# Optimization experiments

Measured on AMD Instinct MI355X. Metric: run time of the kernel, lower is better.

Reference implementation:

```python
import jax, jax.numpy as jnp
import numpy as np

K_STEPS = 10
ALPHA = 0.9
N_NODES = 16384
N_CLASSES = 64
N_EDGES = 524288


def setup_inputs() -> dict:
    key = jax.random.key(0)
    k1, k2, k3 = jax.random.split(key, 3)
    masked_y_true = jax.random.normal(k1, (N_NODES, N_CLASSES), dtype=jnp.float32)
    K = jax.random.normal(k2, (N_NODES, N_NODES), dtype=jnp.float32)
    edge_index = jax.random.randint(k3, (2, N_EDGES), 0, N_NODES, dtype=jnp.int32)
    return {"masked_y_true": masked_y_true, "K": K, "edge_index": edge_index}


def reference(masked_y_true, K, edge_index):
    src, dst = edge_index[0], edge_index[1]
    # DAD normalization: w_e = deg(src)^-1/2 * deg(dst)^-1/2
    deg = jnp.zeros((N_NODES,), jnp.float32).at[dst].add(1.0)
    dinv = jax.lax.rsqrt(jnp.maximum(deg, 1.0))
    w = dinv[src] * dinv[dst]  # [E]

    def spmm(x):
        # A @ x with A in edge-list form (static sparsity, reused each step)
        return jax.ops.segment_sum(w[:, None] * x[src], dst, num_segments=N_NODES)

    def prop_step(_, y):
        return ALPHA * spmm(y) + (1.0 - ALPHA) * y

    y = jax.lax.fori_loop(0, K_STEPS, prop_step, masked_y_true)
    y = K @ y
    y = jax.lax.fori_loop(0, K_STEPS, prop_step, y)
    return y
```

## Files before the change

### kernel.cpp

```cpp
#include <hip/hip_runtime.h>

#define NN 16384
#define NC 64
#define NE 524288
#define ALPHA 0.9f
#define KSTEPS 10

typedef _Float16 f16;
typedef _Float16 f16x4 __attribute__((ext_vector_type(4)));
typedef _Float16 f16x8 __attribute__((ext_vector_type(8)));
typedef float f32x4 __attribute__((ext_vector_type(4)));
typedef int i32x16 __attribute__((ext_vector_type(16)));

#define MEMB   asm volatile("" ::: "memory")
#define SCHED0 __builtin_amdgcn_sched_barrier(0)

__global__ __launch_bounds__(256) void deg_kernel(const int* __restrict__ dst,
                                                  unsigned* __restrict__ deg) {
    int e = blockIdx.x * 256 + threadIdx.x;
    atomicAdd(&deg[dst[e]], 1u);
}

__global__ __launch_bounds__(1024) void scan_kernel(const unsigned* __restrict__ deg,
                                                    float* __restrict__ dinv,
                                                    unsigned* __restrict__ rowoff,
                                                    unsigned* __restrict__ cursor) {
    __shared__ unsigned part[1024];
    const int t = threadIdx.x;
    const int base = t * 16;
    unsigned local[16];
    unsigned s = 0;
    #pragma unroll
    for (int i = 0; i < 16; ++i) {
        local[i] = s;
        s += (deg[base + i] + 15u) & ~15u;
    }
    part[t] = s;
    __syncthreads();
    for (int off = 1; off < 1024; off <<= 1) {
        unsigned v = (t >= off) ? part[t - off] : 0u;
        __syncthreads();
        part[t] += v;
        __syncthreads();
    }
    const unsigned ex = (t == 0) ? 0u : part[t - 1];
    #pragma unroll
    for (int i = 0; i < 16; ++i) {
        unsigned ro = ex + local[i];
        rowoff[base + i] = ro;
        cursor[base + i] = ro;
        unsigned d = deg[base + i];
        dinv[base + i] = rsqrtf(fmaxf((float)d, 1.0f));
    }
    if (t == 1023) rowoff[NN] = part[1023];
}

__global__ __launch_bounds__(256) void fill_kernel(const int* __restrict__ src,
                                                   const int* __restrict__ dst,
                                                   const float* __restrict__ dinv,
                                                   unsigned* __restrict__ cursor,
                                                   int2* __restrict__ csr) {
    int e = blockIdx.x * 256 + threadIdx.x;
    int s = src[e], d = dst[e];
    float w = dinv[s] * dinv[d];
    unsigned p = atomicAdd(&cursor[d], 1u);
    csr[p] = make_int2(s, __float_as_int(w));
}

__global__ __launch_bounds__(256) void prop_kernel(const float* __restrict__ x,
                                                   float* __restrict__ y,
                                                   const unsigned* __restrict__ rowoff,
                                                   const int* __restrict__ csr) {
    const int lane = threadIdx.x & 63;
    const int n = __builtin_amdgcn_readfirstlane(blockIdx.x * 4 + (threadIdx.x >> 6));
    const unsigned beg = rowoff[n];
    const unsigned np = (rowoff[n + 1] - beg) >> 4;
    float acc0 = 0.f, acc1 = 0.f;
    if (np) {
        i32x16 e0 = *(const i32x16*)(csr + 2 * beg);
        i32x16 e1 = *(const i32x16*)(csr + 2 * beg + 16);
        float xv0[8], xv1[8];
        #pragma unroll
        for (int j = 0; j < 8; ++j) xv0[j] = x[(unsigned)e0[2 * j] * 64u + lane];
        #pragma unroll
        for (int j = 0; j < 8; ++j) xv1[j] = x[(unsigned)e1[2 * j] * 64u + lane];
        for (unsigned p = 1; p < np; ++p) {
            const i32x16 f0 = *(const i32x16*)(csr + 2 * (beg + p * 16));
            const i32x16 f1 = *(const i32x16*)(csr + 2 * (beg + p * 16) + 16);
            #pragma unroll
            for (int j = 0; j < 8; ++j) {
                const float w = __int_as_float(e0[2 * j + 1]);
                if (j & 1) acc1 = fmaf(w, xv0[j], acc1);
                else       acc0 = fmaf(w, xv0[j], acc0);
            }
            #pragma unroll
            for (int j = 0; j < 8; ++j) xv0[j] = x[(unsigned)f0[2 * j] * 64u + lane];
            #pragma unroll
            for (int j = 0; j < 8; ++j) {
                const float w = __int_as_float(e1[2 * j + 1]);
                if (j & 1) acc1 = fmaf(w, xv1[j], acc1);
                else       acc0 = fmaf(w, xv1[j], acc0);
            }
            #pragma unroll
            for (int j = 0; j < 8; ++j) xv1[j] = x[(unsigned)f1[2 * j] * 64u + lane];
            e0 = f0; e1 = f1;
        }
        #pragma unroll
        for (int j = 0; j < 8; ++j) {
            const float w = __int_as_float(e0[2 * j + 1]);
            if (j & 1) acc1 = fmaf(w, xv0[j], acc1);
            else       acc0 = fmaf(w, xv0[j], acc0);
        }
        #pragma unroll
        for (int j = 0; j < 8; ++j) {
            const float w = __int_as_float(e1[2 * j + 1]);
            if (j & 1) acc1 = fmaf(w, xv1[j], acc1);
            else       acc0 = fmaf(w, xv1[j], acc0);
        }
    }
    y[n * 64 + lane] = ALPHA * (acc0 + acc1) + (1.0f - ALPHA) * x[n * 64 + lane];
}

__global__ __launch_bounds__(256) void ysplit_kernel(const float* __restrict__ y,
                                                     f16* __restrict__ yhT,
                                                     f16* __restrict__ ylT) {
    __shared__ f16 hb[64][72];
    __shared__ f16 lb[64][72];
    const int t = threadIdx.x;
    const int b = blockIdx.x;
    const int kl = t >> 2;
    const int cq = (t & 3) * 16;
    #pragma unroll
    for (int i = 0; i < 4; ++i) {
        float4 v = *(const float4*)&y[(size_t)(b * 64 + kl) * 64 + cq + i * 4];
        float vv[4] = {v.x, v.y, v.z, v.w};
        #pragma unroll
        for (int j = 0; j < 4; ++j) {
            int c = cq + i * 4 + j;
            f16 h = (f16)vv[j];
            float r = vv[j] - (float)h;
            hb[c][kl] = h;
            lb[c][kl] = (f16)r;
        }
    }
    __syncthreads();
    const int c = t >> 2;
    const int kq = (t & 3) * 16;
    #pragma unroll
    for (int s2 = 0; s2 < 2; ++s2) {
        int slot = (kq >> 3) + s2;
        int dslot = slot ^ (c & 7);
        f16x8 hv, lv;
        #pragma unroll
        for (int j = 0; j < 8; ++j) { hv[j] = hb[c][kq + s2 * 8 + j]; lv[j] = lb[c][kq + s2 * 8 + j]; }
        *(f16x8*)&yhT[(size_t)c * NN + b * 64 + dslot * 8] = hv;
        *(f16x8*)&ylT[(size_t)c * NN + b * 64 + dslot * 8] = lv;
    }
}

__device__ inline void gload16(const void* g, void* l) {
    __builtin_amdgcn_global_load_lds((const __attribute__((address_space(1))) void*)g,
                                     (__attribute__((address_space(3))) void*)l, 16, 0, 0);
}

#define AH_OFF 0
#define AL_OFF 16384
#define YP_OFF 32768

__global__ __launch_bounds__(256, 2) void gemm_kernel(const float* __restrict__ A,
                                                      const f16* __restrict__ yhT,
                                                      const f16* __restrict__ ylT,
                                                      float* __restrict__ z) {
    __shared__ char lds[65536];
    const int t = threadIdx.x;
    const int w = t >> 6;
    const int l = t & 63;
    const size_t row0 = (size_t)blockIdx.x * 128;
    const int kbase = blockIdx.y * 2048;
    const int stag = (blockIdx.x + blockIdx.y * 4) & 31;

    f32x4 acc[2][4];
    #pragma unroll
    for (int m = 0; m < 2; ++m)
        #pragma unroll
        for (int n = 0; n < 4; ++n)
            acc[m][n] = (f32x4){0.f, 0.f, 0.f, 0.f};

    const int arow_l = w * 4 + (l >> 4);
    const int acol = (l & 15) * 4;
    const int ycr = l >> 3;
    const int yco = (l & 7) * 8;

    float4 aA[8], aB[8];

    auto tmap = [&](int tile) { return (stag + tile) & 31; };

    auto loadA = [&](float4 (&dst)[8], int tile) {
        const int kt = kbase + tmap(tile) * 64;
        #pragma unroll
        for (int i = 0; i < 8; ++i)
            dst[i] = *(const float4*)&A[(row0 + i * 16 + arow_l) * 16384 + kt + acol];
    };
    auto issueY = [&](int tile, int cur) {
        const int kt = kbase + tmap(tile) * 64;
        #pragma unroll
        for (int j = 0; j < 2; ++j) {
            const int i = 2 * w + j;
            gload16(yhT + (size_t)(i * 8 + ycr) * NN + kt + yco,
                    lds + YP_OFF + cur * 16384 + i * 1024);
            gload16(ylT + (size_t)(i * 8 + ycr) * NN + kt + yco,
                    lds + YP_OFF + cur * 16384 + 8192 + i * 1024);
        }
    };
    auto writeA = [&](const float4 (&src)[8]) {
        #pragma unroll
        for (int i = 0; i < 8; ++i) {
            const int r = i * 16 + arow_l;
            float v[4] = {src[i].x, src[i].y, src[i].z, src[i].w};
            f16x4 h4, l4;
            #pragma unroll
            for (int j = 0; j < 4; ++j) {
                f16 h = (f16)v[j];
                h4[j] = h;
                l4[j] = (f16)(v[j] - (float)h);
            }
            const int byte = r * 128 + (((((l & 15) >> 1)) ^ (r & 7)) << 4) + (l & 1) * 8;
            *(f16x4*)(lds + AH_OFF + byte) = h4;
            *(f16x4*)(lds + AL_OFF + byte) = l4;
        }
    };
    auto mfmaTile = [&](int cur) {
        #pragma unroll
        for (int s = 0; s < 2; ++s) {
            const int slot = s * 4 + (l >> 4);
            f16x8 ah[2], alo[2];
            #pragma unroll
            for (int m = 0; m < 2; ++m) {
                const int r = w * 32 + m * 16 + (l & 15);
                const int byte = r * 128 + ((slot ^ (r & 7)) << 4);
                ah[m]  = *(const f16x8*)(lds + AH_OFF + byte);
                alo[m] = *(const f16x8*)(lds + AL_OFF + byte);
            }
            #pragma unroll
            for (int n = 0; n < 4; ++n) {
                const int c = n * 16 + (l & 15);
                const int byte = c * 128 + ((slot ^ (c & 7)) << 4);
                const f16x8 bh = *(const f16x8*)(lds + YP_OFF + cur * 16384 + byte);
                const f16x8 bl = *(const f16x8*)(lds + YP_OFF + cur * 16384 + 8192 + byte);
                #pragma unroll
                for (int m = 0; m < 2; ++m) {
                    acc[m][n] = __builtin_amdgcn_mfma_f32_16x16x32_f16(ah[m],  bh, acc[m][n], 0, 0, 0);
                    acc[m][n] = __builtin_amdgcn_mfma_f32_16x16x32_f16(ah[m],  bl, acc[m][n], 0, 0, 0);
                    acc[m][n] = __builtin_amdgcn_mfma_f32_16x16x32_f16(alo[m], bh, acc[m][n], 0, 0, 0);
                }
            }
        }
    };

    loadA(aA, 0); MEMB;
    issueY(0, 0); MEMB;
    loadA(aB, 1); MEMB;
    writeA(aA);
    asm volatile("s_waitcnt vmcnt(8)" ::: "memory");  SCHED0;
    asm volatile("s_waitcnt lgkmcnt(0)" ::: "memory"); SCHED0;
    __builtin_amdgcn_s_barrier(); SCHED0;

#define GEMM_ITER(TILE, CUR, SETF, SETW)                                      \
    issueY((TILE) + 1, (CUR) ^ 1); MEMB;                                      \
    loadA(SETF, (TILE) + 2); MEMB;                                            \
    mfmaTile(CUR);                                                            \
    MEMB; SCHED0;                                                             \
    __builtin_amdgcn_s_barrier();                 \
    writeA(SETW);                                  \
    asm volatile("s_waitcnt vmcnt(8)" ::: "memory");  SCHED0;   \
    asm volatile("s_waitcnt lgkmcnt(0)" ::: "memory"); SCHED0;                \
    __builtin_amdgcn_s_barrier(); SCHED0;

    for (int tp = 0; tp < 15; ++tp) {
        const int t0 = 2 * tp;
        GEMM_ITER(t0,     0, aA, aB);
        GEMM_ITER(t0 + 1, 1, aB, aA);
    }
    issueY(31, 1); MEMB;
    mfmaTile(0);
    MEMB; SCHED0;
    __builtin_amdgcn_s_barrier();
    writeA(aB);
    asm volatile("s_waitcnt vmcnt(0)" ::: "memory");  SCHED0;
    asm volatile("s_waitcnt lgkmcnt(0)" ::: "memory"); SCHED0;
    __builtin_amdgcn_s_barrier(); SCHED0;
    mfmaTile(1);
#undef GEMM_ITER

    #pragma unroll
    for (int m = 0; m < 2; ++m)
        #pragma unroll
        for (int n = 0; n < 4; ++n)
            #pragma unroll
            for (int q = 0; q < 4; ++q) {
                const size_t gr = row0 + w * 32 + m * 16 + (l >> 4) * 4 + q;
                const int gc = n * 16 + (l & 15);
                atomicAdd(&z[gr * 64 + gc], acc[m][n][q]);
            }
}

extern "C" void kernel_launch(void* const* d_in, const int* in_sizes, int n_in,
                              void* d_out, int out_size, void* d_ws, size_t ws_size,
                              hipStream_t stream) {
    const float* ytrue = (const float*)d_in[0];
    const float* Kmat  = (const float*)d_in[1];
    const int*   eidx  = (const int*)d_in[2];
    const int* esrc = eidx;
    const int* edst = eidx + NE;
    float* out = (float*)d_out;

    char* ws = (char*)d_ws;
    size_t off = 0;
    auto alloc = [&](size_t bytes) -> void* {
        void* p = ws + off;
        off += (bytes + 255) & ~(size_t)255;
        return p;
    };
    const size_t CSR_ENTRIES = (size_t)NE + 16 * NN;
    unsigned* deg    = (unsigned*)alloc((size_t)NN * 4);
    unsigned* rowoff = (unsigned*)alloc((size_t)(NN + 1) * 4);
    unsigned* cursor = (unsigned*)alloc((size_t)NN * 4);
    float*    dinv   = (float*)alloc((size_t)NN * 4);
    int2*     csr    = (int2*)alloc(CSR_ENTRIES * 8);
    float*    yA     = (float*)alloc((size_t)NN * NC * 4);
    float*    yB     = (float*)alloc((size_t)NN * NC * 4);
    f16*      yhT    = (f16*)alloc((size_t)NC * NN * 2);
    f16*      ylT    = (f16*)alloc((size_t)NC * NN * 2);

    hipMemsetAsync(deg, 0, (size_t)NN * 4, stream);
    hipMemsetAsync(csr, 0, CSR_ENTRIES * 8, stream);
    deg_kernel<<<NE / 256, 256, 0, stream>>>(edst, deg);
    scan_kernel<<<1, 1024, 0, stream>>>(deg, dinv, rowoff, cursor);
    fill_kernel<<<NE / 256, 256, 0, stream>>>(esrc, edst, dinv, cursor, csr);

    const float* cur = ytrue;
    float* bufs[2] = {yA, yB};
    int pb = 0;
    for (int s = 0; s < KSTEPS; ++s) {
        float* nxt = bufs[pb];
        pb ^= 1;
        prop_kernel<<<NN / 4, 256, 0, stream>>>(cur, nxt, rowoff, (const int*)csr);
        cur = nxt;
    }

    ysplit_kernel<<<NN / 64, 256, 0, stream>>>(cur, yhT, ylT);

    float* z = (cur == yA) ? yB : yA;
    hipMemsetAsync(z, 0, (size_t)NN * NC * 4, stream);
    gemm_kernel<<<dim3(128, 8), 256, 0, stream>>>(Kmat, yhT, ylT, z);

    float* other = (z == yA) ? yB : yA;
    const float* c2 = z;
    for (int s = 0; s < KSTEPS; ++s) {
        float* nxt = (s == KSTEPS - 1) ? out : other;
        prop_kernel<<<NN / 4, 256, 0, stream>>>(c2, nxt, rowoff, (const int*)csr);
        other = (float*)c2;
        c2 = nxt;
    }
}
```

Measured before the change: 522.1 us.

## Load A fragments directly into MFMA registers, skip LDS staging for A

Each wave now loads its own A rows straight from global memory in the MFMA fragment layout and splits fp32 into f16 hi/lo in registers, removing the LDS write/read round trip for A. Only the Y tiles stay in LDS, which halves shared memory use and allows raising the launch-bounds occupancy hint from 2 to 4 blocks. Waves no longer share A loads through LDS, so the per-thread global access pattern changes to 32-byte chunks per row, which may coalesce less well. Register pressure also shifts.

Measured after the change: 550.7 us. 1.05x slower.

```diff
diff --git a/kernel.cpp b/kernel.cpp
--- a/kernel.cpp
+++ b/kernel.cpp
@@ -163,15 +163,11 @@
                                      (__attribute__((address_space(3))) void*)l, 16, 0, 0);
 }
 
-#define AH_OFF 0
-#define AL_OFF 16384
-#define YP_OFF 32768
-
-__global__ __launch_bounds__(256, 2) void gemm_kernel(const float* __restrict__ A,
+__global__ __launch_bounds__(256, 4) void gemm_kernel(const float* __restrict__ A,
                                                       const f16* __restrict__ yhT,
                                                       const f16* __restrict__ ylT,
                                                       float* __restrict__ z) {
-    __shared__ char lds[65536];
+    __shared__ char lds[32768];
     const int t = threadIdx.x;
     const int w = t >> 6;
     const int l = t & 63;
@@ -186,67 +182,58 @@
         for (int n = 0; n < 4; ++n)
             acc[m][n] = (f32x4){0.f, 0.f, 0.f, 0.f};
 
-    const int arow_l = w * 4 + (l >> 4);
-    const int acol = (l & 15) * 4;
     const int ycr = l >> 3;
     const int yco = (l & 7) * 8;
-
-    float4 aA[8], aB[8];
+    const float* abase = A + (row0 + w * 32 + (l & 15)) * 16384 + (l >> 4) * 8;
+
+    float4 rA[2][2][2], rB[2][2][2];
 
     auto tmap = [&](int tile) { return (stag + tile) & 31; };
 
-    auto loadA = [&](float4 (&dst)[8], int tile) {
+    auto loadA = [&](float4 (&dst)[2][2][2], int tile) {
         const int kt = kbase + tmap(tile) * 64;
         #pragma unroll
-        for (int i = 0; i < 8; ++i)
-            dst[i] = *(const float4*)&A[(row0 + i * 16 + arow_l) * 16384 + kt + acol];
+        for (int m = 0; m < 2; ++m)
+            #pragma unroll
+            for (int s = 0; s < 2; ++s) {
+                const float* p = abase + (size_t)m * 16 * 16384 + kt + s * 32;
+                dst[m][s][0] = *(const float4*)p;
+                dst[m][s][1] = *(const float4*)(p + 4);
+            }
     };
-    auto issueY = [&](int tile, int cur) {
+    auto issueY = [&](int tile, int buf) {
         const int kt = kbase + tmap(tile) * 64;
         #pragma unroll
         for (int j = 0; j < 2; ++j) {
             const int i = 2 * w + j;
             gload16(yhT + (size_t)(i * 8 + ycr) * NN + kt + yco,
-                    lds + YP_OFF + cur * 16384 + i * 1024);
+                    lds + buf * 16384 + i * 1024);
             gload16(ylT + (size_t)(i * 8 + ycr) * NN + kt + yco,
-                    lds + YP_OFF + cur * 16384 + 8192 + i * 1024);
+                    lds + buf * 16384 + 8192 + i * 1024);
         }
     };
-    auto writeA = [&](const float4 (&src)[8]) {
-        #pragma unroll
-        for (int i = 0; i < 8; ++i) {
-            const int r = i * 16 + arow_l;
-            float v[4] = {src[i].x, src[i].y, src[i].z, src[i].w};
-            f16x4 h4, l4;
-            #pragma unroll
-            for (int j = 0; j < 4; ++j) {
-                f16 h = (f16)v[j];
-                h4[j] = h;
-                l4[j] = (f16)(v[j] - (float)h);
-            }
-            const int byte = r * 128 + (((((l & 15) >> 1)) ^ (r & 7)) << 4) + (l & 1) * 8;
-            *(f16x4*)(lds + AH_OFF + byte) = h4;
-            *(f16x4*)(lds + AL_OFF + byte) = l4;
-        }
-    };
-    auto mfmaTile = [&](int cur) {
+    auto mfmaTile = [&](const float4 (&raw)[2][2][2], int buf) {
         #pragma unroll
         for (int s = 0; s < 2; ++s) {
             const int slot = s * 4 + (l >> 4);
             f16x8 ah[2], alo[2];
             #pragma unroll
             for (int m = 0; m < 2; ++m) {
-                const int r = w * 32 + m * 16 + (l & 15);
-                const int byte = r * 128 + ((slot ^ (r & 7)) << 4);
-                ah[m]  = *(const f16x8*)(lds + AH_OFF + byte);
-                alo[m] = *(const f16x8*)(lds + AL_OFF + byte);
+                const float vv[8] = {raw[m][s][0].x, raw[m][s][0].y, raw[m][s][0].z, raw[m][s][0].w,
+                                     raw[m][s][1].x, raw[m][s][1].y, raw[m][s][1].z, raw[m][s][1].w};
+                #pragma unroll
+                for (int j = 0; j < 8; ++j) {
+                    f16 h = (f16)vv[j];
+                    ah[m][j] = h;
+                    alo[m][j] = (f16)(vv[j] - (float)h);
+                }
             }
             #pragma unroll
             for (int n = 0; n < 4; ++n) {
                 const int c = n * 16 + (l & 15);
                 const int byte = c * 128 + ((slot ^ (c & 7)) << 4);
-                const f16x8 bh = *(const f16x8*)(lds + YP_OFF + cur * 16384 + byte);
-                const f16x8 bl = *(const f16x8*)(lds + YP_OFF + cur * 16384 + 8192 + byte);
+                const f16x8 bh = *(const f16x8*)(lds + buf * 16384 + byte);
+                const f16x8 bl = *(const f16x8*)(lds + buf * 16384 + 8192 + byte);
                 #pragma unroll
                 for (int m = 0; m < 2; ++m) {
                     acc[m][n] = __builtin_amdgcn_mfma_f32_16x16x32_f16(ah[m],  bh, acc[m][n], 0, 0, 0);
@@ -257,40 +244,31 @@
         }
     };
 
-    loadA(aA, 0); MEMB;
+    loadA(rA, 0); MEMB;
     issueY(0, 0); MEMB;
-    loadA(aB, 1); MEMB;
-    writeA(aA);
-    asm volatile("s_waitcnt vmcnt(8)" ::: "memory");  SCHED0;
-    asm volatile("s_waitcnt lgkmcnt(0)" ::: "memory"); SCHED0;
+    loadA(rB, 1); MEMB;
+    asm volatile("s_waitcnt vmcnt(8)" ::: "memory"); SCHED0;
     __builtin_amdgcn_s_barrier(); SCHED0;
 
-#define GEMM_ITER(TILE, CUR, SETF, SETW)                                      \
-    issueY((TILE) + 1, (CUR) ^ 1); MEMB;                                      \
-    loadA(SETF, (TILE) + 2); MEMB;                                            \
-    mfmaTile(CUR);                                                            \
+#define GEMM_ITER(TILE, SET)                                                  \
+    issueY((TILE) + 1, ((TILE) + 1) & 1); MEMB;                               \
+    mfmaTile(SET, (TILE) & 1);                                                \
     MEMB; SCHED0;                                                             \
-    __builtin_amdgcn_s_barrier();                 \
-    writeA(SETW);                                  \
-    asm volatile("s_waitcnt vmcnt(8)" ::: "memory");  SCHED0;   \
-    asm volatile("s_waitcnt lgkmcnt(0)" ::: "memory"); SCHED0;                \
+    loadA(SET, (TILE) + 2); MEMB;                \
+    asm volatile("s_waitcnt vmcnt(8)" ::: "memory"); SCHED0; \
     __builtin_amdgcn_s_barrier(); SCHED0;
 
     for (int tp = 0; tp < 15; ++tp) {
-        const int t0 = 2 * tp;
-        GEMM_ITER(t0,     0, aA, aB);
-        GEMM_ITER(t0 + 1, 1, aB, aA);
-    }
+        GEMM_ITER(2 * tp,     rA);
+        GEMM_ITER(2 * tp + 1, rB);
+    }
+#undef GEMM_ITER
     issueY(31, 1); MEMB;
-    mfmaTile(0);
+    mfmaTile(rA, 0);
     MEMB; SCHED0;
-    __builtin_amdgcn_s_barrier();
-    writeA(aB);
-    asm volatile("s_waitcnt vmcnt(0)" ::: "memory");  SCHED0;
-    asm volatile("s_waitcnt lgkmcnt(0)" ::: "memory"); SCHED0;
+    asm volatile("s_waitcnt vmcnt(0)" ::: "memory"); SCHED0;
     __builtin_amdgcn_s_barrier(); SCHED0;
-    mfmaTile(1);
-#undef GEMM_ITER
+    mfmaTile(rB, 1);
 
     #pragma unroll
     for (int m = 0; m < 2; ++m)
```
